# Optimization experiments

Hardware: AMD Instinct MI355X
Metric: run time of the kernel (lower is better)

The kernel has to match this reference:

```python
import jax, jax.numpy as jnp
import numpy as np

INP = 64   # inplanes
PLN = 64   # planes
LOC = 64   # loc_planes
EPS = 1e-5


def _linear_init(key, fan_in, fan_out):
    # torch nn.Linear default: U(-1/sqrt(fan_in), 1/sqrt(fan_in)) for W and b
    kw, kb = jax.random.split(key)
    bound = 1.0 / np.sqrt(fan_in)
    W = jax.random.uniform(kw, (fan_in, fan_out), jnp.float32, -bound, bound)
    b = jax.random.uniform(kb, (fan_out,), jnp.float32, -bound, bound)
    return W, b


def setup_inputs() -> dict:
    key = jax.random.key(0)
    ks = jax.random.split(key, 8)
    B, N = 8, 4096
    img_fea = jax.random.normal(ks[0], (B, N, INP), jnp.float32)
    loc_fea = jax.random.normal(ks[1], (B, N, LOC), jnp.float32)
    W11, b11 = _linear_init(ks[2], INP + LOC, INP)
    W12, b12 = _linear_init(ks[3], INP, INP)
    W21, b21 = _linear_init(ks[4], INP + LOC, INP)
    W22, b22 = _linear_init(ks[5], INP, INP * PLN)
    W3, b3 = _linear_init(ks[6], PLN, PLN)
    ln_g = jnp.ones((PLN,), jnp.float32)
    ln_b = jnp.zeros((PLN,), jnp.float32)
    return {
        "img_fea": img_fea, "loc_fea": loc_fea,
        "W11": W11, "b11": b11, "W12": W12, "b12": b12,
        "W21": W21, "b21": b21, "W22": W22, "b22": b22,
        "ln_g": ln_g, "ln_b": ln_b, "W3": W3, "b3": b3,
    }


def reference(img_fea, loc_fea, W11, b11, W12, b12, W21, b21, W22, b22,
              ln_g, ln_b, W3, b3):
    B, N, C = img_fea.shape
    cat_fea = jnp.concatenate([img_fea, loc_fea], axis=2)  # [B,N,INP+LOC]
    # branch 1: per-token input vector
    w11 = jax.nn.relu(cat_fea @ W11 + b11)                 # [B,N,INP]
    w12 = w11 @ W12 + b12                                  # [B,N,INP]
    # branch 2: per-token weight matrix generation
    w21 = jax.nn.relu(cat_fea @ W21 + b21)                 # [B,N,INP]
    w22 = (w21 @ W22 + b22).reshape(B, N, INP, PLN)        # [B,N,INP,PLN]
    # batched tiny matvec: (1,INP) @ (INP,PLN) per token
    x = jnp.einsum('bni,bnio->bno', w12, w22)              # [B,N,PLN]
    # LayerNorm over last dim + ReLU
    mu = jnp.mean(x, axis=-1, keepdims=True)
    var = jnp.mean(jnp.square(x - mu), axis=-1, keepdims=True)
    x = (x - mu) * jax.lax.rsqrt(var + EPS) * ln_g + ln_b
    x = jax.nn.relu(x)
    # final linear (no activation)
    return x @ W3 + b3
```

## Files before the change

kernel.cpp:

```cpp
#include <hip/hip_runtime.h>
#include <cstdint>


typedef __bf16 bf16x4 __attribute__((ext_vector_type(4)));
typedef __bf16 bf16x8 __attribute__((ext_vector_type(8)));
typedef float  f32x4  __attribute__((ext_vector_type(4)));

#define MFMA16(A, B, C) __builtin_amdgcn_mfma_f32_16x16x32_bf16(A, B, C, 0, 0, 0)

#define OFF_BT22 0
#define OFF_W11  266240
#define OFF_W21  274432
#define OFF_W12  282624
#define OFF_W3   286720

__global__ __launch_bounds__(256) void prep_kernel(
    const float* __restrict__ W22, const float* __restrict__ b22,
    const float* __restrict__ W11, const float* __restrict__ W21,
    const float* __restrict__ W12, const float* __restrict__ W3,
    __bf16* __restrict__ ws)
{
    __shared__ __bf16 T[64][72];
    const int b = blockIdx.x, tid = threadIdx.x;
    const float* src; long base = 0;
    if (b < 64)       { src = W22 + b * 4096; }
    else if (b == 64) { src = b22; }
    else if (b < 67)  { src = W11 + (b - 65) * 4096; base = OFF_W11 + (b - 65) * 4096; }
    else if (b < 69)  { src = W21 + (b - 67) * 4096; base = OFF_W21 + (b - 67) * 4096; }
    else if (b == 69) { src = W12;                   base = OFF_W12; }
    else              { src = W3;                    base = OFF_W3; }
    #pragma unroll
    for (int it = 0; it < 4; ++it) {
        int u = it * 1024 + tid * 4;
        int r = u >> 6, c = u & 63;
        const float4 v = *(const float4*)(src + u);
        T[r][c] = (__bf16)v.x; T[r][c + 1] = (__bf16)v.y;
        T[r][c + 2] = (__bf16)v.z; T[r][c + 3] = (__bf16)v.w;
    }
    __syncthreads();
    #pragma unroll
    for (int it = 0; it < 2; ++it) {
        int item = it * 256 + tid;
        int q = item >> 6, o = item & 63;
        bf16x8 pk;
        #pragma unroll
        for (int kj = 0; kj < 8; ++kj) pk[kj] = T[q * 8 + kj][o];
        long dstE;
        if (b <= 64) {
            int k8 = (b == 64 ? 512 : b * 8) + q;
            dstE = OFF_BT22 + ((long)(o >> 4) * 520 + k8) * 128 + (o & 15) * 8;
        } else {
            dstE = base + q * 512 + o * 8;
        }
        *(bf16x8*)(ws + dstE) = pk;
    }
}

#define LOADCH(buf, c) do {                                          \
    buf##_0 = *(const bf16x8*)(Bw + ((c)*16 +  0) * 128);            \
    buf##_1 = *(const bf16x8*)(Bw + ((c)*16 +  4) * 128);            \
    buf##_2 = *(const bf16x8*)(Bw + ((c)*16 +  8) * 128);            \
    buf##_3 = *(const bf16x8*)(Bw + ((c)*16 + 12) * 128);            \
} while (0)

#define COMPUTE_J(b0, b1, j) do {                                    \
    f32x4 w4[4];                                                     \
    _Pragma("unroll")                                                \
    for (int mf = 0; mf < 4; ++mf) {                                 \
        bf16x4 wv4 = *(const bf16x4*)(w21T + (j)*68 + mf*16 + quad*4);\
        w4[mf] = __builtin_convertvector(wv4, f32x4);                \
    }                                                                \
    _Pragma("unroll")                                                \
    for (int mf = 0; mf < 4; ++mf) {                                 \
        f32x4 fz = {};                                               \
        f32x4 m = MFMA16(a12[mf][0], b0, fz);                        \
        m       = MFMA16(a12[mf][1], b1, m);                         \
        _Pragma("unroll")                                            \
        for (int r = 0; r < 4; ++r)                                  \
            acc[mf][r] = fmaf(w4[mf][r], m[r], acc[mf][r]);          \
    }                                                                \
} while (0)

#define COMPUTE(buf, c) do {                                         \
    COMPUTE_J(buf##_0, buf##_1, (c)*2);                              \
    COMPUTE_J(buf##_2, buf##_3, (c)*2 + 1);                          \
} while (0)

__global__ __launch_bounds__(256, 2) void main_kernel(
    const float* __restrict__ img, const float* __restrict__ loc,
    const float* __restrict__ b11, const float* __restrict__ b12,
    const float* __restrict__ b21, const float* __restrict__ ln_g,
    const float* __restrict__ ln_b, const float* __restrict__ b3,
    const __bf16* __restrict__ ws, float* __restrict__ out)
{
    __shared__ __align__(1024) char smem[35328];
    __bf16* catL = (__bf16*)smem;
    __bf16* w12L = (__bf16*)smem;
    float2* ps   = (float2*)(smem + 9216);
    __bf16* w11L = (__bf16*)(smem + 17408);
    __bf16* xL   = w11L;
    __bf16* w21T = (__bf16*)(smem + 26624);

    const int tid  = threadIdx.x;
    const int wv   = tid >> 6;
    const int lane = tid & 63;
    const int ln   = lane & 15;
    const int quad = lane >> 4;
    const int ob   = wv * 16;
    const long tb  = (long)blockIdx.x * 64;

    const __bf16* Bt22  = ws + OFF_BT22;
    const __bf16* W11bt = ws + OFF_W11;
    const __bf16* W21bt = ws + OFF_W21;
    const __bf16* W12bt = ws + OFF_W12;
    const __bf16* W3bt  = ws + OFF_W3;

    {
        const float* srcs[2] = {img, loc};
        #pragma unroll
        for (int s = 0; s < 2; ++s) {
            const float* src = srcs[s] + tb * 64;
            #pragma unroll
            for (int it = 0; it < 4; ++it) {
                int u = (it * 256 + tid) * 4;
                int t = u >> 6, c = u & 63;
                const float4 v = *(const float4*)(src + u);
                bf16x4 pk = {(__bf16)v.x, (__bf16)v.y, (__bf16)v.z, (__bf16)v.w};
                *(bf16x4*)(catL + t * 136 + s * 64 + c) = pk;
            }
        }
    }
    __syncthreads();

    {
        const int isW21 = wv >> 1;
        const int cb0 = (wv & 1) * 32;
        const __bf16* Wbt = isW21 ? W21bt : W11bt;
        const float* bsel = isW21 ? b21 : b11;
        f32x4 a1[4][2] = {};
        #pragma unroll
        for (int kb = 0; kb < 4; ++kb) {
            bf16x8 af[4];
            #pragma unroll
            for (int mf = 0; mf < 4; ++mf)
                af[mf] = *(const bf16x8*)(catL + (mf*16 + ln)*136 + kb*32 + quad*8);
            #pragma unroll
            for (int nf = 0; nf < 2; ++nf) {
                bf16x8 bw = *(const bf16x8*)(Wbt + ((kb*4 + quad)*64 + cb0 + nf*16 + ln)*8);
                #pragma unroll
                for (int mf = 0; mf < 4; ++mf)
                    a1[mf][nf] = MFMA16(af[mf], bw, a1[mf][nf]);
            }
        }
        if (!isW21) {
            #pragma unroll
            for (int nf = 0; nf < 2; ++nf) {
                int o = cb0 + nf*16 + ln;
                float cb = bsel[o];
                #pragma unroll
                for (int mf = 0; mf < 4; ++mf)
                    #pragma unroll
                    for (int r = 0; r < 4; ++r) {
                        int t = mf*16 + quad*4 + r;
                        float v = a1[mf][nf][r] + cb; v = v > 0.f ? v : 0.f;
                        w11L[t*72 + o] = (__bf16)v;
                    }
            }
        } else {
            #pragma unroll
            for (int nf = 0; nf < 2; ++nf) {
                int o = cb0 + nf*16 + ln;
                float cb = bsel[o];
                #pragma unroll
                for (int mf = 0; mf < 4; ++mf) {
                    bf16x4 pk;
                    #pragma unroll
                    for (int r = 0; r < 4; ++r) {
                        float v = a1[mf][nf][r] + cb; v = v > 0.f ? v : 0.f;
                        pk[r] = (__bf16)v;
                    }
                    *(bf16x4*)(w21T + o*68 + mf*16 + quad*4) = pk;
                }
            }
        }
    }
    __syncthreads();

    {
        float c12 = b12[ob + ln];
        f32x4 a12c[4] = {};
        #pragma unroll
        for (int kb = 0; kb < 2; ++kb) {
            bf16x8 bw = *(const bf16x8*)(W12bt + ((kb*4 + quad)*64 + ob + ln)*8);
            #pragma unroll
            for (int mf = 0; mf < 4; ++mf) {
                bf16x8 af = *(const bf16x8*)(w11L + (mf*16 + ln)*72 + kb*32 + quad*8);
                a12c[mf] = MFMA16(af, bw, a12c[mf]);
            }
        }
        #pragma unroll
        for (int mf = 0; mf < 4; ++mf)
            #pragma unroll
            for (int r = 0; r < 4; ++r) {
                int t = mf*16 + quad*4 + r;
                w12L[t*72 + ob + ln] = (__bf16)(a12c[mf][r] + c12);
            }
    }
    __syncthreads();

    bf16x8 a12[4][2];
    #pragma unroll
    for (int mf = 0; mf < 4; ++mf)
        #pragma unroll
        for (int sub = 0; sub < 2; ++sub)
            a12[mf][sub] = *(const bf16x8*)(w12L + (mf*16 + ln)*72 + sub*32 + quad*8);

    const __bf16* Bw = Bt22 + ((long)wv * 520 + quad) * 128 + ln * 8;

    bf16x8 B0_0, B0_1, B0_2, B0_3;
    bf16x8 B1_0, B1_1, B1_2, B1_3;

    f32x4 acc[4] = {};
    LOADCH(B0, 0);
    #pragma unroll 1
    for (int cc = 0; cc < 32; cc += 2) {
        LOADCH(B1, cc + 1);
        COMPUTE(B0, cc);
        if (cc + 2 < 32) LOADCH(B0, cc + 2);
        COMPUTE(B1, cc + 1);
    }
    {
        bf16x8 bb0 = *(const bf16x8*)(Bw + (512 + 0) * 128);
        bf16x8 bb1 = *(const bf16x8*)(Bw + (512 + 4) * 128);
        #pragma unroll
        for (int mf = 0; mf < 4; ++mf) {
            acc[mf] = MFMA16(a12[mf][0], bb0, acc[mf]);
            acc[mf] = MFMA16(a12[mf][1], bb1, acc[mf]);
        }
    }

    #pragma unroll
    for (int mf = 0; mf < 4; ++mf)
        #pragma unroll
        for (int r = 0; r < 4; ++r) {
            float v = acc[mf][r];
            float s1 = v, s2 = v*v;
            #pragma unroll
            for (int d = 1; d < 16; d <<= 1) {
                s1 += __shfl_xor(s1, d, 64);
                s2 += __shfl_xor(s2, d, 64);
            }
            if (ln == 0) {
                int t = mf*16 + quad*4 + r;
                ps[t*4 + wv] = make_float2(s1, s2);
            }
        }
    __syncthreads();

    float gv = ln_g[ob + ln], bv = ln_b[ob + ln], b3v = b3[ob + ln];
    #pragma unroll
    for (int mf = 0; mf < 4; ++mf)
        #pragma unroll
        for (int r = 0; r < 4; ++r) {
            int t = mf*16 + quad*4 + r;
            float2 p0 = ps[t*4], p1 = ps[t*4 + 1], p2 = ps[t*4 + 2], p3 = ps[t*4 + 3];
            float mean = (p0.x + p1.x + p2.x + p3.x) * 0.015625f;
            float var  = (p0.y + p1.y + p2.y + p3.y) * 0.015625f - mean * mean;
            float inv  = rsqrtf(var + 1e-5f);
            float v = (acc[mf][r] - mean) * inv * gv + bv;
            v = v > 0.f ? v : 0.f;
            xL[t*72 + ob + ln] = (__bf16)v;
        }
    __syncthreads();

    f32x4 a3[4] = {};
    #pragma unroll
    for (int kb = 0; kb < 2; ++kb) {
        bf16x8 bfr = *(const bf16x8*)(W3bt + ((kb*4 + quad)*64 + ob + ln)*8);
        #pragma unroll
        for (int mf = 0; mf < 4; ++mf) {
            bf16x8 af = *(const bf16x8*)(xL + (mf*16 + ln)*72 + kb*32 + quad*8);
            a3[mf] = MFMA16(af, bfr, a3[mf]);
        }
    }
    #pragma unroll
    for (int mf = 0; mf < 4; ++mf)
        #pragma unroll
        for (int r = 0; r < 4; ++r) {
            long t = tb + mf*16 + quad*4 + r;
            out[t*64 + ob + ln] = a3[mf][r] + b3v;
        }
}

extern "C" void kernel_launch(void* const* d_in, const int* in_sizes, int n_in,
                              void* d_out, int out_size, void* d_ws, size_t ws_size,
                              hipStream_t stream)
{
    const float* img  = (const float*)d_in[0];
    const float* loc  = (const float*)d_in[1];
    const float* W11  = (const float*)d_in[2];
    const float* b11  = (const float*)d_in[3];
    const float* W12  = (const float*)d_in[4];
    const float* b12  = (const float*)d_in[5];
    const float* W21  = (const float*)d_in[6];
    const float* b21  = (const float*)d_in[7];
    const float* W22  = (const float*)d_in[8];
    const float* b22  = (const float*)d_in[9];
    const float* ln_g = (const float*)d_in[10];
    const float* ln_b = (const float*)d_in[11];
    const float* W3   = (const float*)d_in[12];
    const float* b3   = (const float*)d_in[13];
    __bf16* ws = (__bf16*)d_ws;
    float*  o  = (float*)d_out;

    prep_kernel<<<71, 256, 0, stream>>>(W22, b22, W11, W21, W12, W3, ws);
    main_kernel<<<512, 256, 0, stream>>>(img, loc, b11, b12, b21, ln_g, ln_b, b3, ws, o);
}
```

Baseline: 116.9 us.

## Double block tile to 128 tokens with 512 threads sharing W22 stream

Each block now processes 128 tokens with 8 waves, where pairs of waves take the same output-column group for different 64-token halves. Two waves in a block thus read the same W22 slices, which may improve cache reuse and halves the number of blocks. Shared memory roughly doubles to about 70 KB. With 256 blocks of 512 threads there are fewer blocks than needed to fill all CUs twice on a 256-CU part, which risks lower occupancy and load balance.

```diff
diff --git a/kernel.cpp b/kernel.cpp
--- a/kernel.cpp
+++ b/kernel.cpp
@@ -67,7 +67,7 @@
     f32x4 w4[4];                                                     \
     _Pragma("unroll")                                                \
     for (int mf = 0; mf < 4; ++mf) {                                 \
-        bf16x4 wv4 = *(const bf16x4*)(w21T + (j)*68 + mf*16 + quad*4);\
+        bf16x4 wv4 = *(const bf16x4*)(w21T + (j)*132 + wt + mf*16 + quad*4);\
         w4[mf] = __builtin_convertvector(wv4, f32x4);                \
     }                                                                \
     _Pragma("unroll")                                                \
@@ -86,28 +86,31 @@
     COMPUTE_J(buf##_2, buf##_3, (c)*2 + 1);                          \
 } while (0)
 
-__global__ __launch_bounds__(256, 2) void main_kernel(
+__global__ __launch_bounds__(512, 2) void main_kernel(
     const float* __restrict__ img, const float* __restrict__ loc,
     const float* __restrict__ b11, const float* __restrict__ b12,
     const float* __restrict__ b21, const float* __restrict__ ln_g,
     const float* __restrict__ ln_b, const float* __restrict__ b3,
     const __bf16* __restrict__ ws, float* __restrict__ out)
 {
-    __shared__ __align__(1024) char smem[35328];
+    __shared__ __align__(1024) char smem[70144];
     __bf16* catL = (__bf16*)smem;
     __bf16* w12L = (__bf16*)smem;
-    float2* ps   = (float2*)(smem + 9216);
-    __bf16* w11L = (__bf16*)(smem + 17408);
+    float2* ps   = (float2*)(smem + 18432);
+    __bf16* w11L = (__bf16*)(smem + 34816);
     __bf16* xL   = w11L;
-    __bf16* w21T = (__bf16*)(smem + 26624);
+    __bf16* w21T = (__bf16*)(smem + 53248);
 
     const int tid  = threadIdx.x;
     const int wv   = tid >> 6;
     const int lane = tid & 63;
     const int ln   = lane & 15;
     const int quad = lane >> 4;
-    const int ob   = wv * 16;
-    const long tb  = (long)blockIdx.x * 64;
+    const int th   = wv & 1;
+    const int og   = wv >> 1;
+    const int wt   = th * 64;
+    const int ob   = og * 16;
+    const long tb  = (long)blockIdx.x * 128;
 
     const __bf16* Bt22  = ws + OFF_BT22;
     const __bf16* W11bt = ws + OFF_W11;
@@ -122,7 +125,7 @@
             const float* src = srcs[s] + tb * 64;
             #pragma unroll
             for (int it = 0; it < 4; ++it) {
-                int u = (it * 256 + tid) * 4;
+                int u = (it * 512 + tid) * 4;
                 int t = u >> 6, c = u & 63;
                 const float4 v = *(const float4*)(src + u);
                 bf16x4 pk = {(__bf16)v.x, (__bf16)v.y, (__bf16)v.z, (__bf16)v.w};
@@ -133,8 +136,11 @@
     __syncthreads();
 
     {
-        const int isW21 = wv >> 1;
-        const int cb0 = (wv & 1) * 32;
+        const int isW21 = wv >> 2;
+        const int w     = wv & 3;
+        const int th1   = w >> 1;
+        const int cb0   = (w & 1) * 32;
+        const int wt1   = th1 * 64;
         const __bf16* Wbt = isW21 ? W21bt : W11bt;
         const float* bsel = isW21 ? b21 : b11;
         f32x4 a1[4][2] = {};
@@ -143,7 +149,7 @@
             bf16x8 af[4];
             #pragma unroll
             for (int mf = 0; mf < 4; ++mf)
-                af[mf] = *(const bf16x8*)(catL + (mf*16 + ln)*136 + kb*32 + quad*8);
+                af[mf] = *(const bf16x8*)(catL + (wt1 + mf*16 + ln)*136 + kb*32 + quad*8);
             #pragma unroll
             for (int nf = 0; nf < 2; ++nf) {
                 bf16x8 bw = *(const bf16x8*)(Wbt + ((kb*4 + quad)*64 + cb0 + nf*16 + ln)*8);
@@ -161,7 +167,7 @@
                 for (int mf = 0; mf < 4; ++mf)
                     #pragma unroll
                     for (int r = 0; r < 4; ++r) {
-                        int t = mf*16 + quad*4 + r;
+                        int t = wt1 + mf*16 + quad*4 + r;
                         float v = a1[mf][nf][r] + cb; v = v > 0.f ? v : 0.f;
                         w11L[t*72 + o] = (__bf16)v;
                     }
@@ -179,7 +185,7 @@
                         float v = a1[mf][nf][r] + cb; v = v > 0.f ? v : 0.f;
                         pk[r] = (__bf16)v;
                     }
-                    *(bf16x4*)(w21T + o*68 + mf*16 + quad*4) = pk;
+                    *(bf16x4*)(w21T + o*132 + wt1 + mf*16 + quad*4) = pk;
                 }
             }
         }
@@ -194,7 +200,7 @@
             bf16x8 bw = *(const bf16x8*)(W12bt + ((kb*4 + quad)*64 + ob + ln)*8);
             #pragma unroll
             for (int mf = 0; mf < 4; ++mf) {
-                bf16x8 af = *(const bf16x8*)(w11L + (mf*16 + ln)*72 + kb*32 + quad*8);
+                bf16x8 af = *(const bf16x8*)(w11L + (wt + mf*16 + ln)*72 + kb*32 + quad*8);
                 a12c[mf] = MFMA16(af, bw, a12c[mf]);
             }
         }
@@ -202,7 +208,7 @@
         for (int mf = 0; mf < 4; ++mf)
             #pragma unroll
             for (int r = 0; r < 4; ++r) {
-                int t = mf*16 + quad*4 + r;
+                int t = wt + mf*16 + quad*4 + r;
                 w12L[t*72 + ob + ln] = (__bf16)(a12c[mf][r] + c12);
             }
     }
@@ -213,9 +219,9 @@
     for (int mf = 0; mf < 4; ++mf)
         #pragma unroll
         for (int sub = 0; sub < 2; ++sub)
-            a12[mf][sub] = *(const bf16x8*)(w12L + (mf*16 + ln)*72 + sub*32 + quad*8);
-
-    const __bf16* Bw = Bt22 + ((long)wv * 520 + quad) * 128 + ln * 8;
+            a12[mf][sub] = *(const bf16x8*)(w12L + (wt + mf*16 + ln)*72 + sub*32 + quad*8);
+
+    const __bf16* Bw = Bt22 + ((long)og * 520 + quad) * 128 + ln * 8;
 
     bf16x8 B0_0, B0_1, B0_2, B0_3;
     bf16x8 B1_0, B1_1, B1_2, B1_3;
@@ -251,8 +257,8 @@
                 s2 += __shfl_xor(s2, d, 64);
             }
             if (ln == 0) {
-                int t = mf*16 + quad*4 + r;
-                ps[t*4 + wv] = make_float2(s1, s2);
+                int t = wt + mf*16 + quad*4 + r;
+                ps[t*4 + og] = make_float2(s1, s2);
             }
         }
     __syncthreads();
@@ -262,7 +268,7 @@
     for (int mf = 0; mf < 4; ++mf)
         #pragma unroll
         for (int r = 0; r < 4; ++r) {
-            int t = mf*16 + quad*4 + r;
+            int t = wt + mf*16 + quad*4 + r;
             float2 p0 = ps[t*4], p1 = ps[t*4 + 1], p2 = ps[t*4 + 2], p3 = ps[t*4 + 3];
             float mean = (p0.x + p1.x + p2.x + p3.x) * 0.015625f;
             float var  = (p0.y + p1.y + p2.y + p3.y) * 0.015625f - mean * mean;
@@ -279,7 +285,7 @@
         bf16x8 bfr = *(const bf16x8*)(W3bt + ((kb*4 + quad)*64 + ob + ln)*8);
         #pragma unroll
         for (int mf = 0; mf < 4; ++mf) {
-            bf16x8 af = *(const bf16x8*)(xL + (mf*16 + ln)*72 + kb*32 + quad*8);
+            bf16x8 af = *(const bf16x8*)(xL + (wt + mf*16 + ln)*72 + kb*32 + quad*8);
             a3[mf] = MFMA16(af, bfr, a3[mf]);
         }
     }
@@ -287,7 +293,7 @@
     for (int mf = 0; mf < 4; ++mf)
         #pragma unroll
         for (int r = 0; r < 4; ++r) {
-            long t = tb + mf*16 + quad*4 + r;
+            long t = tb + wt + mf*16 + quad*4 + r;
             out[t*64 + ob + ln] = a3[mf][r] + b3v;
         }
 }
@@ -314,5 +320,5 @@
     float*  o  = (float*)d_out;
 
     prep_kernel<<<71, 256, 0, stream>>>(W22, b22, W11, W21, W12, W3, ws);
-    main_kernel<<<512, 256, 0, stream>>>(img, loc, b11, b12, b21, ln_g, ln_b, b3, ws, o);
+    main_kernel<<<256, 512, 0, stream>>>(img, loc, b11, b12, b21, ln_g, ln_b, b3, ws, o);
 }
```

Result: no change. 115.5 us (-1.2%).
